# Optimization experiments

Measured on AMD Instinct MI355X. Metric: run time of the kernel, lower is better.

Reference implementation:

```python
import jax, jax.numpy as jnp
import numpy as np

HIDDEN = 2048
NUM_HEADS = 32
NUM_KV_HEADS = 8
HEAD_DIM = HIDDEN // NUM_HEADS  # 64
GROUP = NUM_HEADS // NUM_KV_HEADS  # 4
B, S = 2, 2048


def setup_inputs() -> dict:
    key = jax.random.key(0)
    ks = jax.random.split(key, 9)
    sc = 0.02
    kv_dim = NUM_KV_HEADS * HEAD_DIM
    return {
        "x": jax.random.normal(ks[0], (B, S, HIDDEN), jnp.float32),
        # weights stored as [in, out] (transpose of torch Linear.weight)
        "Wq": jax.random.normal(ks[1], (HIDDEN, HIDDEN), jnp.float32) * sc,
        "bq": jnp.zeros((HIDDEN,), jnp.float32),
        "Wk": jax.random.normal(ks[2], (HIDDEN, kv_dim), jnp.float32) * sc,
        "bk": jnp.zeros((kv_dim,), jnp.float32),
        "Wv": jax.random.normal(ks[3], (HIDDEN, kv_dim), jnp.float32) * sc,
        "bv": jnp.zeros((kv_dim,), jnp.float32),
        "Wo": jax.random.normal(ks[4], (HIDDEN, HIDDEN), jnp.float32) * sc,
        "bo": jnp.zeros((HIDDEN,), jnp.float32),
    }


def reference(x, Wq, bq, Wk, bk, Wv, bv, Wo, bo):
    b, s, _ = x.shape
    q = (x @ Wq + bq).reshape(b, s, NUM_KV_HEADS, GROUP, HEAD_DIM)
    k = (x @ Wk + bk).reshape(b, s, NUM_KV_HEADS, HEAD_DIM)
    v = (x @ Wv + bv).reshape(b, s, NUM_KV_HEADS, HEAD_DIM)
    scale = 1.0 / jnp.sqrt(jnp.asarray(HEAD_DIM, x.dtype))
    # scores: [b, g(kv heads), r(q per group), s(query), t(key)]
    scores = jnp.einsum("bsgrd,btgd->bgrst", q, k) * scale
    attn = jax.nn.softmax(scores, axis=-1)  # dropout rate 0 -> identity
    out = jnp.einsum("bgrst,btgd->bsgrd", attn, v).reshape(b, s, HIDDEN)
    return out @ Wo + bo
```

## Files before the change

kernel.cpp:

```cpp
#include <hip/hip_runtime.h>

#define HIDDEN 2048
#define NHEADS 32
#define NKV 8
#define HD 64
#define BATCH 2
#define SEQ 2048
#define KVD 512
#define BSZ 4096
#define QKVD 3072

typedef __bf16 bfx8 __attribute__((ext_vector_type(8)));
typedef __bf16 bfx4 __attribute__((ext_vector_type(4)));
typedef float f32x4 __attribute__((ext_vector_type(4)));
typedef short sx4v __attribute__((ext_vector_type(4)));

#define QSCALE 0.1803368801111204f

#if defined(__AMDGCN__) && __has_builtin(__builtin_amdgcn_mfma_f32_16x16x16_bf16)
#define MFMA16(a, b, c) __builtin_amdgcn_mfma_f32_16x16x16_bf16(a, b, c, 0, 0, 0)
#else
#define MFMA16(a, b, c)                                                    \
    __builtin_amdgcn_mfma_f32_16x16x16bf16_1k(__builtin_bit_cast(sx4v, (a)), \
                                              __builtin_bit_cast(sx4v, (b)), (c), 0, 0, 0)
#endif

__device__ __forceinline__ void gl_lds16(const __bf16* g, __bf16* l) {
    __builtin_amdgcn_global_load_lds(
        (const __attribute__((address_space(1))) unsigned int*)g,
        (__attribute__((address_space(3))) unsigned int*)l, 16, 0, 0);
}

__global__ __launch_bounds__(256) void cvt_bf16(const float* __restrict__ src,
                                                __bf16* __restrict__ dst, int n4) {
    int i = blockIdx.x * 256 + threadIdx.x;
    if (i >= n4) return;
    float4 f = ((const float4*)src)[i];
    bfx4 o = {(__bf16)f.x, (__bf16)f.y, (__bf16)f.z, (__bf16)f.w};
    *(bfx4*)(dst + (size_t)i * 4) = o;
}

__device__ __forceinline__ void tcvt_tile(const float* __restrict__ src,
                                          __bf16* __restrict__ dst,
                                          int R, int C, int tx, int ty,
                                          float (*tile)[65], int t, float mul) {
    int br = ty * 64, bc = tx * 64;
    {
        int r = t >> 4, c = (t & 15) * 4;
#pragma unroll
        for (int i = 0; i < 4; ++i) {
            float4 v = *(const float4*)(&src[(long)(br + r + i * 16) * C + bc + c]);
            tile[r + i * 16][c + 0] = v.x * mul;
            tile[r + i * 16][c + 1] = v.y * mul;
            tile[r + i * 16][c + 2] = v.z * mul;
            tile[r + i * 16][c + 3] = v.w * mul;
        }
    }
    __syncthreads();
    {
        int d = t >> 2, tt0 = (t & 3) * 16;
        bfx8 o0, o1;
#pragma unroll
        for (int j = 0; j < 8; ++j) o0[j] = (__bf16)tile[tt0 + j][d];
#pragma unroll
        for (int j = 0; j < 8; ++j) o1[j] = (__bf16)tile[tt0 + 8 + j][d];
        *(bfx8*)(&dst[(long)(bc + d) * R + br + tt0]) = o0;
        *(bfx8*)(&dst[(long)(bc + d) * R + br + tt0 + 8]) = o1;
    }
}

__global__ __launch_bounds__(256) void prep(const float* __restrict__ Wq,
                                            const float* __restrict__ Wk,
                                            const float* __restrict__ Wv,
                                            const float* __restrict__ Wo,
                                            const float* __restrict__ bq,
                                            const float* __restrict__ bk,
                                            const float* __restrict__ bv,
                                            __bf16* __restrict__ wqkvt,
                                            __bf16* __restrict__ wot,
                                            float* __restrict__ bqkv) {
    __shared__ float tile[64][65];
    int idx = blockIdx.x, t = threadIdx.x;
    if (idx < 1024) {
        tcvt_tile(Wq, wqkvt, HIDDEN, HIDDEN, idx & 31, idx >> 5, tile, t, QSCALE);
    } else if (idx < 1280) {
        int l = idx - 1024;
        tcvt_tile(Wk, wqkvt + (size_t)HIDDEN * HIDDEN, HIDDEN, KVD, l & 7, l >> 3, tile, t, 1.0f);
    } else if (idx < 1536) {
        int l = idx - 1280;
        tcvt_tile(Wv, wqkvt + (size_t)(HIDDEN + KVD) * HIDDEN, HIDDEN, KVD, l & 7, l >> 3, tile, t, 1.0f);
    } else if (idx < 2560) {
        int l = idx - 1536;
        tcvt_tile(Wo, wot, HIDDEN, HIDDEN, l & 31, l >> 5, tile, t, 1.0f);
    } else {
        int i = (idx - 2560) * 256 + t;
        if (i < QKVD) {
            float v = (i < HIDDEN) ? bq[i] * QSCALE
                                   : (i < HIDDEN + KVD ? bk[i - HIDDEN] : bv[i - HIDDEN - KVD]);
            bqkv[i] = v;
        }
    }
}

__global__ __launch_bounds__(256) void transpose_v(const __bf16* __restrict__ qkv,
                                                   __bf16* __restrict__ vt) {
    __shared__ __bf16 tile[64][65];
    int t = threadIdx.x;
    int nb0 = blockIdx.x * 64;
    int bh = blockIdx.y;
    int b = bh >> 3, kv = bh & 7;
    {
        int tt = t >> 2, c0 = (t & 3) * 16;
        const __bf16* p = &qkv[(long)(b * SEQ + nb0 + tt) * QKVD + HIDDEN + KVD + kv * HD + c0];
        bfx8 a0 = *(const bfx8*)(p);
        bfx8 a1 = *(const bfx8*)(p + 8);
#pragma unroll
        for (int j = 0; j < 8; ++j) tile[tt][c0 + j] = a0[j];
#pragma unroll
        for (int j = 0; j < 8; ++j) tile[tt][c0 + 8 + j] = a1[j];
    }
    __syncthreads();
    {
        int d = t >> 2, tt0 = (t & 3) * 16;
        bfx8 o0, o1;
#pragma unroll
        for (int j = 0; j < 8; ++j) o0[j] = tile[tt0 + j][d];
#pragma unroll
        for (int j = 0; j < 8; ++j) o1[j] = tile[tt0 + 8 + j][d];
        __bf16* q = &vt[((long)bh * HD + d) * SEQ + nb0 + tt0];
        *(bfx8*)(q) = o0;
        *(bfx8*)(q + 8) = o1;
    }
}

template <bool OUT_BF16>
__global__ __launch_bounds__(256, 3) void gemm128(const __bf16* __restrict__ A,
                                                  const __bf16* __restrict__ Bt,
                                                  const float* __restrict__ bias,
                                                  void* __restrict__ C,
                                                  int M, int N, int K) {
    __shared__ __align__(16) __bf16 As[2][128 * 32];
    __shared__ __align__(16) __bf16 Bs[2][128 * 32];
    int t = threadIdx.x;
    int w = t >> 6, lane = t & 63;
    int lrow = lane & 15, quad = lane >> 4;
    long m0 = (long)blockIdx.y * 128, n0 = (long)blockIdx.x * 128;
    int wr = (w >> 1) * 64, wc = (w & 1) * 64;
    f32x4 acc[4][4] = {};
    int srow = t >> 2, scol = (((t & 3) ^ ((t >> 3) & 3))) * 8;
    int sA = (lrow >> 1) & 3;
    const __bf16* Ag = A + (m0 + srow) * (long)K + scol;
    const __bf16* Bg = Bt + (n0 + srow) * (long)K + scol;
#define STAGE_G(kb, buf)                                                      \
    {                                                                         \
        _Pragma("unroll") for (int c = 0; c < 2; ++c) {                       \
            gl_lds16(Ag + (long)c * 64 * K + (kb), &As[buf][c * 2048 + w * 512]); \
            gl_lds16(Bg + (long)c * 64 * K + (kb), &Bs[buf][c * 2048 + w * 512]); \
        }                                                                     \
    }
    STAGE_G(0, 0);
    int nk = K >> 5;
    for (int it = 0; it < nk; ++it) {
        __syncthreads();
        if (it + 1 < nk) STAGE_G((it + 1) * 32, (it + 1) & 1);
        const __bf16* Ab = &As[it & 1][0];
        const __bf16* Bb = &Bs[it & 1][0];
        bfx8 af[4], bfr[4];
#pragma unroll
        for (int i = 0; i < 4; ++i)
            af[i] = *(const bfx8*)&Ab[(wr + i * 16 + lrow) * 32 + ((quad ^ sA) * 8)];
#pragma unroll
        for (int j = 0; j < 4; ++j)
            bfr[j] = *(const bfx8*)&Bb[(wc + j * 16 + lrow) * 32 + ((quad ^ sA) * 8)];
#pragma unroll
        for (int i = 0; i < 4; ++i)
#pragma unroll
            for (int j = 0; j < 4; ++j)
                acc[i][j] = __builtin_amdgcn_mfma_f32_16x16x32_bf16(af[i], bfr[j], acc[i][j], 0, 0, 0);
    }
#undef STAGE_G
#pragma unroll
    for (int j = 0; j < 4; ++j) {
        long col = n0 + wc + j * 16 + lrow;
        float bv = bias[col];
#pragma unroll
        for (int i = 0; i < 4; ++i) {
#pragma unroll
            for (int r = 0; r < 4; ++r) {
                long row = m0 + wr + i * 16 + quad * 4 + r;
                float val = acc[i][j][r] + bv;
                if (OUT_BF16)
                    ((__bf16*)C)[row * N + col] = (__bf16)val;
                else
                    ((float*)C)[row * N + col] = val;
            }
        }
    }
}

__global__ __launch_bounds__(256, 2) void attn(const __bf16* __restrict__ QKV,
                                               const __bf16* __restrict__ Vt,
                                               __bf16* __restrict__ O) {
    __shared__ __align__(16) __bf16 Ks[2][64 * 64];
    __shared__ __align__(16) __bf16 Vs[2][64 * 64];
    int t = threadIdx.x;
    int w = t >> 6, lane = t & 63;
    int lrow = lane & 15, quad = lane >> 4;
    int qb = blockIdx.x, bh = blockIdx.y;
    int b = bh >> 5, h = bh & 31, kv = h >> 2;
    int q0 = qb * 256 + w * 64;

    bfx8 qf[4][2];
#pragma unroll
    for (int i = 0; i < 4; ++i)
#pragma unroll
        for (int kk = 0; kk < 2; ++kk)
            qf[i][kk] = *(const bfx8*)(QKV + (long)(b * SEQ + q0 + i * 16 + lrow) * QKVD +
                                       h * HD + kk * 32 + quad * 8);

    int srow = t >> 2, scol = (((t & 3) ^ ((t >> 3) & 3))) * 8;
    int sA = (lrow >> 1) & 3;
    const __bf16* kg = QKV + (long)(b * SEQ + srow) * QKVD + HIDDEN + kv * HD + scol;
    const __bf16* vg = Vt + ((long)(b * NKV + kv) * HD + srow) * SEQ + scol;
#define STAGE_KV(nb, buf)                                                          \
    {                                                                              \
        _Pragma("unroll") for (int c = 0; c < 2; ++c) {                            \
            gl_lds16(kg + (long)(nb)*QKVD + c * 32, &Ks[buf][c * 2048 + w * 512]); \
            gl_lds16(vg + (nb) + c * 32, &Vs[buf][c * 2048 + w * 512]);            \
        }                                                                          \
    }
    STAGE_KV(0, 0);

    f32x4 accO[4][4] = {};
    float lacc[4] = {0.f, 0.f, 0.f, 0.f};

    for (int it = 0; it < SEQ / 64; ++it) {
        __syncthreads();
        if (it + 1 < SEQ / 64) STAGE_KV((it + 1) * 64, (it + 1) & 1);
        const __bf16* Kb = &Ks[it & 1][0];
        const __bf16* Vb = &Vs[it & 1][0];
#pragma unroll
        for (int tt = 0; tt < 4; ++tt) {
            bfx8 ka0 = *(const bfx8*)&Kb[tt * 512 + lrow * 32 + ((quad ^ sA) * 8)];
            bfx8 ka1 = *(const bfx8*)&Kb[2048 + tt * 512 + lrow * 32 + ((quad ^ sA) * 8)];
            f32x4 s2[4];
#pragma unroll
            for (int i = 0; i < 4; ++i) {
                f32x4 z = {};
                z = __builtin_amdgcn_mfma_f32_16x16x32_bf16(ka0, qf[i][0], z, 0, 0, 0);
                s2[i] = __builtin_amdgcn_mfma_f32_16x16x32_bf16(ka1, qf[i][1], z, 0, 0, 0);
            }
            bfx4 pb[4];
#pragma unroll
            for (int i = 0; i < 4; ++i) {
                float p0 = __builtin_amdgcn_exp2f(s2[i][0]);
                float p1 = __builtin_amdgcn_exp2f(s2[i][1]);
                float p2 = __builtin_amdgcn_exp2f(s2[i][2]);
                float p3 = __builtin_amdgcn_exp2f(s2[i][3]);
                lacc[i] += (p0 + p1) + (p2 + p3);
                bfx4 pp = {(__bf16)p0, (__bf16)p1, (__bf16)p2, (__bf16)p3};
                pb[i] = pp;
            }
            int vbase = (tt >> 1) * 2048 + lrow * 32 +
                        ((((tt & 1) * 2 + (quad >> 1)) ^ sA) * 8) + (quad & 1) * 4;
#pragma unroll
            for (int dt = 0; dt < 4; ++dt) {
                bfx4 va = *(const bfx4*)&Vb[vbase + dt * 512];
#pragma unroll
                for (int i = 0; i < 4; ++i)
                    accO[dt][i] = MFMA16(va, pb[i], accO[dt][i]);
            }
        }
    }
    float inv[4];
#pragma unroll
    for (int i = 0; i < 4; ++i) {
        float l = lacc[i];
        l += __shfl_xor(l, 16);
        l += __shfl_xor(l, 32);
        inv[i] = 1.0f / l;
    }
#pragma unroll
    for (int i = 0; i < 4; ++i) {
        long row = (long)(b * SEQ + q0 + i * 16 + lrow);
#pragma unroll
        for (int dt = 0; dt < 4; ++dt) {
            bfx4 o4 = {(__bf16)(accO[dt][i][0] * inv[i]), (__bf16)(accO[dt][i][1] * inv[i]),
                       (__bf16)(accO[dt][i][2] * inv[i]), (__bf16)(accO[dt][i][3] * inv[i])};
            *(bfx4*)&O[row * HIDDEN + h * HD + dt * 16 + quad * 4] = o4;
        }
    }
#undef STAGE_KV
}

extern "C" void kernel_launch(void* const* d_in, const int* in_sizes, int n_in,
                              void* d_out, int out_size, void* d_ws, size_t ws_size,
                              hipStream_t stream) {
    const float* x  = (const float*)d_in[0];
    const float* Wq = (const float*)d_in[1];
    const float* bq = (const float*)d_in[2];
    const float* Wk = (const float*)d_in[3];
    const float* bk = (const float*)d_in[4];
    const float* Wv = (const float*)d_in[5];
    const float* bv = (const float*)d_in[6];
    const float* Wo = (const float*)d_in[7];
    const float* bo = (const float*)d_in[8];
    float* out = (float*)d_out;

    __bf16* ws    = (__bf16*)d_ws;
    __bf16* xb    = ws;
    __bf16* wqkvt = xb + (size_t)BSZ * HIDDEN;
    __bf16* wot   = wqkvt + (size_t)QKVD * HIDDEN;
    __bf16* qkv   = wot + (size_t)HIDDEN * HIDDEN;
    __bf16* vt_   = qkv + (size_t)BSZ * QKVD;
    __bf16* ab_   = vt_ + (size_t)BSZ * KVD;
    float*  bqkv  = (float*)(ab_ + (size_t)BSZ * HIDDEN);

    cvt_bf16<<<(BSZ * HIDDEN / 4 + 255) / 256, 256, 0, stream>>>(x, xb, BSZ * HIDDEN / 4);
    prep<<<2560 + (QKVD + 255) / 256, 256, 0, stream>>>(Wq, Wk, Wv, Wo, bq, bk, bv,
                                                        wqkvt, wot, bqkv);

    gemm128<true><<<dim3(QKVD / 128, BSZ / 128), 256, 0, stream>>>(xb, wqkvt, bqkv, qkv, BSZ, QKVD, HIDDEN);

    transpose_v<<<dim3(SEQ / 64, BATCH * NKV), 256, 0, stream>>>(qkv, vt_);
    attn<<<dim3(SEQ / 256, BATCH * NHEADS), 256, 0, stream>>>(qkv, vt_, ab_);

    gemm128<false><<<dim3(HIDDEN / 128, BSZ / 128), 256, 0, stream>>>(ab_, wot, bo, out, BSZ, HIDDEN, HIDDEN);
}
```

Baseline: 318.4 us.

## Use 16x16x32 MFMA for PV with permlane swaps to repack probabilities

```diff
diff --git a/kernel.cpp b/kernel.cpp
--- a/kernel.cpp
+++ b/kernel.cpp
@@ -12,23 +12,21 @@
 
 typedef __bf16 bfx8 __attribute__((ext_vector_type(8)));
 typedef __bf16 bfx4 __attribute__((ext_vector_type(4)));
+typedef __bf16 bfx2 __attribute__((ext_vector_type(2)));
 typedef float f32x4 __attribute__((ext_vector_type(4)));
-typedef short sx4v __attribute__((ext_vector_type(4)));
+typedef unsigned int ux4 __attribute__((ext_vector_type(4)));
 
 #define QSCALE 0.1803368801111204f
-
-#if defined(__AMDGCN__) && __has_builtin(__builtin_amdgcn_mfma_f32_16x16x16_bf16)
-#define MFMA16(a, b, c) __builtin_amdgcn_mfma_f32_16x16x16_bf16(a, b, c, 0, 0, 0)
-#else
-#define MFMA16(a, b, c)                                                    \
-    __builtin_amdgcn_mfma_f32_16x16x16bf16_1k(__builtin_bit_cast(sx4v, (a)), \
-                                              __builtin_bit_cast(sx4v, (b)), (c), 0, 0, 0)
-#endif
 
 __device__ __forceinline__ void gl_lds16(const __bf16* g, __bf16* l) {
     __builtin_amdgcn_global_load_lds(
         (const __attribute__((address_space(1))) unsigned int*)g,
         (__attribute__((address_space(3))) unsigned int*)l, 16, 0, 0);
+}
+
+__device__ __forceinline__ unsigned int pk2(float lo, float hi) {
+    bfx2 v = {(__bf16)lo, (__bf16)hi};
+    return __builtin_bit_cast(unsigned int, v);
 }
 
 __global__ __launch_bounds__(256) void cvt_bf16(const float* __restrict__ src,
@@ -240,35 +238,43 @@
         const __bf16* Kb = &Ks[it & 1][0];
         const __bf16* Vb = &Vs[it & 1][0];
 #pragma unroll
-        for (int tt = 0; tt < 4; ++tt) {
-            bfx8 ka0 = *(const bfx8*)&Kb[tt * 512 + lrow * 32 + ((quad ^ sA) * 8)];
-            bfx8 ka1 = *(const bfx8*)&Kb[2048 + tt * 512 + lrow * 32 + ((quad ^ sA) * 8)];
-            f32x4 s2[4];
+        for (int ch = 0; ch < 2; ++ch) {
+            int rcol = (quad ^ sA) * 8;
+            bfx8 ka0a = *(const bfx8*)&Kb[(2 * ch + 0) * 512 + lrow * 32 + rcol];
+            bfx8 ka1a = *(const bfx8*)&Kb[2048 + (2 * ch + 0) * 512 + lrow * 32 + rcol];
+            bfx8 ka0b = *(const bfx8*)&Kb[(2 * ch + 1) * 512 + lrow * 32 + rcol];
+            bfx8 ka1b = *(const bfx8*)&Kb[2048 + (2 * ch + 1) * 512 + lrow * 32 + rcol];
+            bfx8 va[4];
+#pragma unroll
+            for (int dt = 0; dt < 4; ++dt)
+                va[dt] = *(const bfx8*)&Vb[ch * 2048 + (dt * 16 + lrow) * 32 + rcol];
 #pragma unroll
             for (int i = 0; i < 4; ++i) {
-                f32x4 z = {};
-                z = __builtin_amdgcn_mfma_f32_16x16x32_bf16(ka0, qf[i][0], z, 0, 0, 0);
-                s2[i] = __builtin_amdgcn_mfma_f32_16x16x32_bf16(ka1, qf[i][1], z, 0, 0, 0);
-            }
-            bfx4 pb[4];
-#pragma unroll
-            for (int i = 0; i < 4; ++i) {
-                float p0 = __builtin_amdgcn_exp2f(s2[i][0]);
-                float p1 = __builtin_amdgcn_exp2f(s2[i][1]);
-                float p2 = __builtin_amdgcn_exp2f(s2[i][2]);
-                float p3 = __builtin_amdgcn_exp2f(s2[i][3]);
-                lacc[i] += (p0 + p1) + (p2 + p3);
-                bfx4 pp = {(__bf16)p0, (__bf16)p1, (__bf16)p2, (__bf16)p3};
-                pb[i] = pp;
-            }
-            int vbase = (tt >> 1) * 2048 + lrow * 32 +
-                        ((((tt & 1) * 2 + (quad >> 1)) ^ sA) * 8) + (quad & 1) * 4;
-#pragma unroll
-            for (int dt = 0; dt < 4; ++dt) {
-                bfx4 va = *(const bfx4*)&Vb[vbase + dt * 512];
-#pragma unroll
-                for (int i = 0; i < 4; ++i)
-                    accO[dt][i] = MFMA16(va, pb[i], accO[dt][i]);
+                f32x4 za = {}, zb = {};
+                za = __builtin_amdgcn_mfma_f32_16x16x32_bf16(ka0a, qf[i][0], za, 0, 0, 0);
+                zb = __builtin_amdgcn_mfma_f32_16x16x32_bf16(ka0b, qf[i][0], zb, 0, 0, 0);
+                f32x4 sa = __builtin_amdgcn_mfma_f32_16x16x32_bf16(ka1a, qf[i][1], za, 0, 0, 0);
+                f32x4 sb = __builtin_amdgcn_mfma_f32_16x16x32_bf16(ka1b, qf[i][1], zb, 0, 0, 0);
+                float pa0 = __builtin_amdgcn_exp2f(sa[0]);
+                float pa1 = __builtin_amdgcn_exp2f(sa[1]);
+                float pa2 = __builtin_amdgcn_exp2f(sa[2]);
+                float pa3 = __builtin_amdgcn_exp2f(sa[3]);
+                float pb0 = __builtin_amdgcn_exp2f(sb[0]);
+                float pb1 = __builtin_amdgcn_exp2f(sb[1]);
+                float pb2 = __builtin_amdgcn_exp2f(sb[2]);
+                float pb3 = __builtin_amdgcn_exp2f(sb[3]);
+                lacc[i] += ((pa0 + pa1) + (pa2 + pa3)) + ((pb0 + pb1) + (pb2 + pb3));
+                unsigned int A0 = pk2(pa0, pa1), A1 = pk2(pa2, pa3);
+                unsigned int B0 = pk2(pb0, pb1), B1 = pk2(pb2, pb3);
+                asm volatile("v_permlane32_swap_b32 %0, %1" : "+v"(A0), "+v"(B0));
+                asm volatile("v_permlane16_swap_b32 %0, %1" : "+v"(A0), "+v"(B0));
+                asm volatile("v_permlane32_swap_b32 %0, %1" : "+v"(A1), "+v"(B1));
+                asm volatile("v_permlane16_swap_b32 %0, %1" : "+v"(A1), "+v"(B1));
+                ux4 pw = {A0, A1, B0, B1};
+                bfx8 p8 = __builtin_bit_cast(bfx8, pw);
+#pragma unroll
+                for (int dt = 0; dt < 4; ++dt)
+                    accO[dt][i] = __builtin_amdgcn_mfma_f32_16x16x32_bf16(va[dt], p8, accO[dt][i], 0, 0, 0);
             }
         }
     }
```

Result: no change. 318.9 us (+0.2%).
